# Optimization experiments

Hardware: AMD Instinct MI355X
Metric: run time of the kernel (lower is better)

The kernel has to match this reference:

```python
import jax, jax.numpy as jnp
import numpy as np

B, T, S = 512, 2048, 24
START, STOP = 22, 23
NEG = -10000.0


def setup_inputs() -> dict:
    key = jax.random.key(0)
    k1, k2, k3, k4 = jax.random.split(key, 4)
    feats = jax.random.normal(k1, (B, T, S), dtype=jnp.float32)
    transitions = jax.random.normal(k2, (S, S), dtype=jnp.float32)
    # match torch __init__: no transition INTO START, none OUT OF STOP
    transitions = transitions.at[START, :].set(NEG).at[:, STOP].set(NEG)
    tags = jax.random.randint(k3, (B, T), 0, START)          # gold tags exclude START/STOP
    lengths = jax.random.randint(k4, (B,), 1, T + 1)         # true lengths in [1, T]
    return {"feats": feats, "transitions": transitions, "tags": tags, "lengths": lengths}


def reference(feats, transitions, tags, lengths):
    Bb, Tt, Ss = feats.shape
    mask = jnp.arange(Tt)[None, :] < lengths[:, None]  # (B, T) valid-step mask

    # ---- forward algorithm (log partition) ----
    init = jnp.full((Bb, Ss), NEG, dtype=feats.dtype).at[:, START].set(0.0)

    def step(fv, xs):
        feat_t, m_t = xs  # (B, S), (B,)
        # score[b, next, prev] = fv[b, prev] + trans[next, prev]; logsumexp over prev
        nxt = jax.nn.logsumexp(fv[:, None, :] + transitions[None, :, :], axis=2) + feat_t
        fv_new = jnp.where(m_t[:, None], nxt, fv)
        return fv_new, None

    fv, _ = jax.lax.scan(step, init, (feats.transpose(1, 0, 2), mask.T))
    alpha = jax.nn.logsumexp(fv + transitions[STOP][None, :], axis=1)  # (B,)

    # ---- gold sequence score ----
    start_col = jnp.full((Bb, 1), START, dtype=tags.dtype)
    ext = jnp.concatenate([start_col, tags], axis=1)  # (B, T+1)
    cur, prev = ext[:, 1:], ext[:, :-1]
    trans_s = transitions[cur, prev]                                  # (B, T)
    emit_s = jnp.take_along_axis(feats, cur[:, :, None], axis=2)[..., 0]  # (B, T)
    last_tags = jnp.take_along_axis(tags, (lengths - 1)[:, None], axis=1)[:, 0]
    gold = jnp.sum(jnp.where(mask, trans_s + emit_s, 0.0), axis=1) + transitions[STOP, last_tags]

    return jnp.mean(alpha - gold)
```

## Files before the change

kernel.cpp:

```cpp
#include <hip/hip_runtime.h>
#include <math.h>

#define NBATCH 512
#define TLEN   2048
#define NS     24
#define KSTART 22
#define KSTOP  23
#define MID    1024
#define L2E    1.4426950408889634f
#define LN2F   0.6931471805599453f

__device__ __forceinline__ float fexp2(float x) {
#if __has_builtin(__builtin_amdgcn_exp2f)
  return __builtin_amdgcn_exp2f(x);
#else
  return exp2f(x);
#endif
}
__device__ __forceinline__ float flog2(float x) {
#if __has_builtin(__builtin_amdgcn_logf)
  return __builtin_amdgcn_logf(x);
#else
  return __log2f(x);
#endif
}

__device__ __forceinline__ float rl(float v, int k) {
  return __int_as_float(__builtin_amdgcn_readlane(__float_as_int(v), k));
}

#define SWZ(X, IMM) __int_as_float(__builtin_amdgcn_ds_swizzle(__float_as_int(X), (IMM)))

template<bool ISB>
__device__ __forceinline__ void run_chain(
    const float* __restrict__ fb, const float* __restrict__ trans,
    int steps, int lenm1, int j, int je,
    float* __restrict__ outg, float* __restrict__ outc)
{
  const bool act = (j < NS);

  float p[NS];
  #pragma unroll
  for (int k = 0; k < NS; ++k) {
    int idx = ISB ? (k * NS + je) : (je * NS + k);
    float tv = trans[idx];
    p[k] = act ? fexp2(tv * L2E) : 0.0f;
  }

  float g;
  if (ISB) g = act ? fexp2(trans[KSTOP * NS + je] * L2E) : 0.0f;
  else     g = (j == KSTART) ? 1.0f : 0.0f;
  int cE = 0;

  auto ldf = [&](int k) -> float {
    int t = ISB ? (lenm1 - k) : k;
    t = (t < 0) ? 0 : t;
    return fb[t * NS + je];
  };

#define DOT24(SRC) \
  y0 = p[0]*rl(SRC,0);             y1 = p[1]*rl(SRC,1);             y2 = p[2]*rl(SRC,2);             y3 = p[3]*rl(SRC,3); \
  y0 = fmaf(p[4],  rl(SRC,4),  y0); y1 = fmaf(p[5],  rl(SRC,5),  y1); y2 = fmaf(p[6],  rl(SRC,6),  y2); y3 = fmaf(p[7],  rl(SRC,7),  y3); \
  y0 = fmaf(p[8],  rl(SRC,8),  y0); y1 = fmaf(p[9],  rl(SRC,9),  y1); y2 = fmaf(p[10], rl(SRC,10), y2); y3 = fmaf(p[11], rl(SRC,11), y3); \
  y0 = fmaf(p[12], rl(SRC,12), y0); y1 = fmaf(p[13], rl(SRC,13), y1); y2 = fmaf(p[14], rl(SRC,14), y2); y3 = fmaf(p[15], rl(SRC,15), y3); \
  y0 = fmaf(p[16], rl(SRC,16), y0); y1 = fmaf(p[17], rl(SRC,17), y1); y2 = fmaf(p[18], rl(SRC,18), y2); y3 = fmaf(p[19], rl(SRC,19), y3); \
  y0 = fmaf(p[20], rl(SRC,20), y0); y1 = fmaf(p[21], rl(SRC,21), y1); y2 = fmaf(p[22], rl(SRC,22), y2); y3 = fmaf(p[23], rl(SRC,23), y3);

#define STEP1(EU) { float y0, y1, y2, y3; \
    if constexpr (ISB) { float m = g * (EU); DOT24(m); g = (y0 + y1) + (y2 + y3); } \
    else               { DOT24(g); g = ((y0 + y1) + (y2 + y3)) * (EU); } }

#define RENORM { int b0_ = __builtin_amdgcn_readlane(__float_as_int(g), 0); \
    int er_ = (b0_ >> 23) & 0xFF; int E_ = (er_ == 0) ? 0 : (er_ - 127); \
    cE += E_; g *= __int_as_float((127 - E_) << 23); }

  float f0 = ldf(0), f1 = ldf(1), f2 = ldf(2), f3 = ldf(3),
        f4 = ldf(4), f5 = ldf(5), f6 = ldf(6), f7 = ldf(7);
  float e0 = fexp2(f0 * L2E), e1 = fexp2(f1 * L2E), e2 = fexp2(f2 * L2E), e3 = fexp2(f3 * L2E),
        e4 = fexp2(f4 * L2E), e5 = fexp2(f5 * L2E), e6 = fexp2(f6 * L2E), e7 = fexp2(f7 * L2E);
  f0 = ldf(8);  f1 = ldf(9);  f2 = ldf(10); f3 = ldf(11);
  f4 = ldf(12); f5 = ldf(13); f6 = ldf(14); f7 = ldf(15);

  int k0 = 0;
  for (; k0 + 8 <= steps; k0 += 8) {
    float n0 = ldf(k0 + 16), n1 = ldf(k0 + 17), n2 = ldf(k0 + 18), n3 = ldf(k0 + 19),
          n4 = ldf(k0 + 20), n5 = ldf(k0 + 21), n6 = ldf(k0 + 22), n7 = ldf(k0 + 23);
    float x0 = fexp2(f0 * L2E), x1 = fexp2(f1 * L2E), x2 = fexp2(f2 * L2E), x3 = fexp2(f3 * L2E),
          x4 = fexp2(f4 * L2E), x5 = fexp2(f5 * L2E), x6 = fexp2(f6 * L2E), x7 = fexp2(f7 * L2E);
    STEP1(e0) STEP1(e1) STEP1(e2) STEP1(e3)
    RENORM
    STEP1(e4) STEP1(e5) STEP1(e6) STEP1(e7)
    RENORM
    f0 = n0; f1 = n1; f2 = n2; f3 = n3; f4 = n4; f5 = n5; f6 = n6; f7 = n7;
    e0 = x0; e1 = x1; e2 = x2; e3 = x3; e4 = x4; e5 = x5; e6 = x6; e7 = x7;
  }
  int r = steps - k0;
  if (r > 0) STEP1(e0)
  if (r > 1) STEP1(e1)
  if (r > 2) STEP1(e2)
  if (r > 3) STEP1(e3)
  if (r > 4) { RENORM STEP1(e4) }
  if (r > 5) STEP1(e5)
  if (r > 6) STEP1(e6)
  RENORM

  if (act) outg[j] = g;
  if (j == 0) *outc = (float)cE;

#undef DOT24
#undef STEP1
#undef RENORM
}

__global__ __launch_bounds__(128) void crf_chains(
    const float* __restrict__ feats, const float* __restrict__ trans,
    const int* __restrict__ lengths, float* __restrict__ acc)
{
  __shared__ float shg[2][NS];
  __shared__ float shc[2];
  const int b   = blockIdx.x;
  const int tid = threadIdx.x;
  const int dir = tid >> 6;
  const int j   = tid & 63;
  const int je  = (j < NS) ? j : (NS - 1);
  const int len = lengths[b];
  const int lenm1 = len - 1;
  const float* fb = feats + (size_t)b * (TLEN * NS);

  if (dir == 0) {
    int fsteps = (len < MID) ? len : MID;
    run_chain<false>(fb, trans, fsteps, lenm1, j, je, shg[0], &shc[0]);
  } else {
    int bsteps = (len > MID) ? (len - MID) : 0;
    run_chain<true>(fb, trans, bsteps, lenm1, j, je, shg[1], &shc[1]);
  }
  __syncthreads();

  if (tid < 32) {
    float prod = (tid < NS) ? shg[0][tid] * shg[1][tid] : 0.0f;
    prod += SWZ(prod, 0x041F);
    prod += SWZ(prod, 0x081F);
    prod += SWZ(prod, 0x101F);
    prod += SWZ(prod, 0x201F);
    prod += SWZ(prod, 0x401F);
    if (tid == 0) {
      float alpha2 = shc[0] + shc[1] + flog2(prod);
      atomicAdd(acc, alpha2 * LN2F);
    }
  }
}

__global__ __launch_bounds__(256) void crf_gold(
    const float* __restrict__ feats, const float* __restrict__ trans,
    const int* __restrict__ tags, const int* __restrict__ lengths,
    float* __restrict__ acc)
{
  const int b   = blockIdx.x;
  const int tid = threadIdx.x;
  const int len = lengths[b];
  const int* tg = tags + (size_t)b * TLEN;
  const float* fb = feats + (size_t)b * (TLEN * NS);

  float s = 0.0f;
  for (int t = tid; t < len; t += 256) {
    int cur  = tg[t];
    int prev = (t == 0) ? KSTART : tg[t - 1];
    s += trans[cur * NS + prev] + fb[t * NS + cur];
  }
  if (tid == 0) s += trans[KSTOP * NS + tg[len - 1]];
  s = -s;
  s += SWZ(s, 0x041F);
  s += SWZ(s, 0x081F);
  s += SWZ(s, 0x101F);
  s += SWZ(s, 0x201F);
  s += SWZ(s, 0x401F);
  if ((tid & 31) == 0) atomicAdd(acc, s);
}

__global__ void crf_final(float* out) {
  out[0] = out[0] * (1.0f / (float)NBATCH);
}

extern "C" void kernel_launch(void* const* d_in, const int* in_sizes, int n_in,
                              void* d_out, int out_size, void* d_ws, size_t ws_size,
                              hipStream_t stream) {
  const float* feats   = (const float*)d_in[0];
  const float* trans   = (const float*)d_in[1];
  const int*   tags    = (const int*)d_in[2];
  const int*   lengths = (const int*)d_in[3];
  float* out = (float*)d_out;

  hipMemsetAsync(out, 0, sizeof(float), stream);
  crf_chains<<<NBATCH, 128, 0, stream>>>(feats, trans, lengths, out);
  crf_gold<<<NBATCH, 256, 0, stream>>>(feats, trans, tags, lengths, out);
  crf_final<<<1, 1, 0, stream>>>(out);
}
```

Measured before the change: 345.4 us.

## Replace atomics with workspace reduction, split gold scoring, hoist readlanes

The chain and gold kernels now write per-batch partial sums into a workspace, and the final kernel reduces them. This removes the memset and the float atomics, and makes the result deterministic. The gold kernel is split into four chunks per batch so more blocks run, and its reduction now goes through shared memory. The chain DOT24 hoists all 24 readlanes ahead of the FMAs and adds a waves_per_eu hint, to give the scheduler more freedom at the possible cost of extra register pressure.

```diff
diff --git a/kernel.cpp b/kernel.cpp
--- a/kernel.cpp
+++ b/kernel.cpp
@@ -10,6 +10,10 @@
 #define L2E    1.4426950408889634f
 #define LN2F   0.6931471805599453f
 
+#define GOLD_CHUNKS 4
+#define GOLD_CLEN   (TLEN / GOLD_CHUNKS)
+#define WS_TOTAL    (NBATCH + NBATCH * GOLD_CHUNKS)
+
 __device__ __forceinline__ float fexp2(float x) {
 #if __has_builtin(__builtin_amdgcn_exp2f)
   return __builtin_amdgcn_exp2f(x);
@@ -59,12 +63,18 @@
   };
 
 #define DOT24(SRC) \
-  y0 = p[0]*rl(SRC,0);             y1 = p[1]*rl(SRC,1);             y2 = p[2]*rl(SRC,2);             y3 = p[3]*rl(SRC,3); \
-  y0 = fmaf(p[4],  rl(SRC,4),  y0); y1 = fmaf(p[5],  rl(SRC,5),  y1); y2 = fmaf(p[6],  rl(SRC,6),  y2); y3 = fmaf(p[7],  rl(SRC,7),  y3); \
-  y0 = fmaf(p[8],  rl(SRC,8),  y0); y1 = fmaf(p[9],  rl(SRC,9),  y1); y2 = fmaf(p[10], rl(SRC,10), y2); y3 = fmaf(p[11], rl(SRC,11), y3); \
-  y0 = fmaf(p[12], rl(SRC,12), y0); y1 = fmaf(p[13], rl(SRC,13), y1); y2 = fmaf(p[14], rl(SRC,14), y2); y3 = fmaf(p[15], rl(SRC,15), y3); \
-  y0 = fmaf(p[16], rl(SRC,16), y0); y1 = fmaf(p[17], rl(SRC,17), y1); y2 = fmaf(p[18], rl(SRC,18), y2); y3 = fmaf(p[19], rl(SRC,19), y3); \
-  y0 = fmaf(p[20], rl(SRC,20), y0); y1 = fmaf(p[21], rl(SRC,21), y1); y2 = fmaf(p[22], rl(SRC,22), y2); y3 = fmaf(p[23], rl(SRC,23), y3);
+  const float s0  = rl(SRC, 0),  s1  = rl(SRC, 1),  s2  = rl(SRC, 2),  s3  = rl(SRC, 3),  \
+              s4  = rl(SRC, 4),  s5  = rl(SRC, 5),  s6  = rl(SRC, 6),  s7  = rl(SRC, 7),  \
+              s8  = rl(SRC, 8),  s9  = rl(SRC, 9),  s10 = rl(SRC, 10), s11 = rl(SRC, 11), \
+              s12 = rl(SRC, 12), s13 = rl(SRC, 13), s14 = rl(SRC, 14), s15 = rl(SRC, 15), \
+              s16 = rl(SRC, 16), s17 = rl(SRC, 17), s18 = rl(SRC, 18), s19 = rl(SRC, 19), \
+              s20 = rl(SRC, 20), s21 = rl(SRC, 21), s22 = rl(SRC, 22), s23 = rl(SRC, 23); \
+  y0 = p[0] * s0;              y1 = p[1] * s1;              y2 = p[2] * s2;              y3 = p[3] * s3; \
+  y0 = fmaf(p[4],  s4,  y0);   y1 = fmaf(p[5],  s5,  y1);   y2 = fmaf(p[6],  s6,  y2);   y3 = fmaf(p[7],  s7,  y3); \
+  y0 = fmaf(p[8],  s8,  y0);   y1 = fmaf(p[9],  s9,  y1);   y2 = fmaf(p[10], s10, y2);   y3 = fmaf(p[11], s11, y3); \
+  y0 = fmaf(p[12], s12, y0);   y1 = fmaf(p[13], s13, y1);   y2 = fmaf(p[14], s14, y2);   y3 = fmaf(p[15], s15, y3); \
+  y0 = fmaf(p[16], s16, y0);   y1 = fmaf(p[17], s17, y1);   y2 = fmaf(p[18], s18, y2);   y3 = fmaf(p[19], s19, y3); \
+  y0 = fmaf(p[20], s20, y0);   y1 = fmaf(p[21], s21, y1);   y2 = fmaf(p[22], s22, y2);   y3 = fmaf(p[23], s23, y3);
 
 #define STEP1(EU) { float y0, y1, y2, y3; \
     if constexpr (ISB) { float m = g * (EU); DOT24(m); g = (y0 + y1) + (y2 + y3); } \
@@ -112,9 +122,10 @@
 #undef RENORM
 }
 
-__global__ __launch_bounds__(128) void crf_chains(
+__global__ __launch_bounds__(128) __attribute__((amdgpu_waves_per_eu(1, 2)))
+void crf_chains(
     const float* __restrict__ feats, const float* __restrict__ trans,
-    const int* __restrict__ lengths, float* __restrict__ acc)
+    const int* __restrict__ lengths, float* __restrict__ ws)
 {
   __shared__ float shg[2][NS];
   __shared__ float shc[2];
@@ -145,7 +156,7 @@
     prod += SWZ(prod, 0x401F);
     if (tid == 0) {
       float alpha2 = shc[0] + shc[1] + flog2(prod);
-      atomicAdd(acc, alpha2 * LN2F);
+      ws[b] = alpha2 * LN2F;
     }
   }
 }
@@ -153,32 +164,56 @@
 __global__ __launch_bounds__(256) void crf_gold(
     const float* __restrict__ feats, const float* __restrict__ trans,
     const int* __restrict__ tags, const int* __restrict__ lengths,
-    float* __restrict__ acc)
-{
-  const int b   = blockIdx.x;
+    float* __restrict__ ws)
+{
+  const int blk = blockIdx.x;
+  const int b   = blk >> 2;
+  const int c   = blk & 3;
   const int tid = threadIdx.x;
   const int len = lengths[b];
   const int* tg = tags + (size_t)b * TLEN;
   const float* fb = feats + (size_t)b * (TLEN * NS);
 
+  const int t0 = c * GOLD_CLEN + tid;
+  const int t1 = t0 + 256;
+
   float s = 0.0f;
-  for (int t = tid; t < len; t += 256) {
-    int cur  = tg[t];
-    int prev = (t == 0) ? KSTART : tg[t - 1];
-    s += trans[cur * NS + prev] + fb[t * NS + cur];
-  }
-  if (tid == 0) s += trans[KSTOP * NS + tg[len - 1]];
-  s = -s;
-  s += SWZ(s, 0x041F);
-  s += SWZ(s, 0x081F);
-  s += SWZ(s, 0x101F);
-  s += SWZ(s, 0x201F);
-  s += SWZ(s, 0x401F);
-  if ((tid & 31) == 0) atomicAdd(acc, s);
-}
-
-__global__ void crf_final(float* out) {
-  out[0] = out[0] * (1.0f / (float)NBATCH);
+  if (t0 < len) {
+    int cur  = tg[t0];
+    int prev = (t0 == 0) ? KSTART : tg[t0 - 1];
+    s += trans[cur * NS + prev] + fb[t0 * NS + cur];
+  }
+  if (t1 < len) {
+    int cur  = tg[t1];
+    int prev = tg[t1 - 1];
+    s += trans[cur * NS + prev] + fb[t1 * NS + cur];
+  }
+  if (c == 0 && tid == 0) s += trans[KSTOP * NS + tg[len - 1]];
+
+  __shared__ float red[256];
+  red[tid] = s;
+  __syncthreads();
+  for (int off = 128; off > 0; off >>= 1) {
+    if (tid < off) red[tid] += red[tid + off];
+    __syncthreads();
+  }
+  if (tid == 0) ws[NBATCH + blk] = -red[0];
+}
+
+__global__ __launch_bounds__(256) void crf_final(const float* __restrict__ ws,
+                                                 float* __restrict__ out)
+{
+  const int tid = threadIdx.x;
+  float s = 0.0f;
+  for (int i = tid; i < WS_TOTAL; i += 256) s += ws[i];
+  __shared__ float red[256];
+  red[tid] = s;
+  __syncthreads();
+  for (int off = 128; off > 0; off >>= 1) {
+    if (tid < off) red[tid] += red[tid + off];
+    __syncthreads();
+  }
+  if (tid == 0) out[0] = red[0] * (1.0f / (float)NBATCH);
 }
 
 extern "C" void kernel_launch(void* const* d_in, const int* in_sizes, int n_in,
@@ -189,9 +224,9 @@
   const int*   tags    = (const int*)d_in[2];
   const int*   lengths = (const int*)d_in[3];
   float* out = (float*)d_out;
-
-  hipMemsetAsync(out, 0, sizeof(float), stream);
-  crf_chains<<<NBATCH, 128, 0, stream>>>(feats, trans, lengths, out);
-  crf_gold<<<NBATCH, 256, 0, stream>>>(feats, trans, tags, lengths, out);
-  crf_final<<<1, 1, 0, stream>>>(out);
-}
+  float* ws  = (float*)d_ws;
+
+  crf_chains<<<NBATCH, 128, 0, stream>>>(feats, trans, lengths, ws);
+  crf_gold<<<NBATCH * GOLD_CHUNKS, 256, 0, stream>>>(feats, trans, tags, lengths, ws);
+  crf_final<<<1, 256, 0, stream>>>(ws, out);
+}
```

Result: faster. 331.6 us (-4.0%).
